# Kernel optimization log

Hardware: AMD Instinct MI355X
Metric: run time of the kernel (lower is better)

The kernel has to match this reference:

```python
import jax, jax.numpy as jnp
import numpy as np

DIN = 256
N_RATIOS = 3          # cfg.ANCHOR_RATIOS = [0.5, 1, 2]
NC_SCORE = N_RATIOS * 2   # 6
NC_BBOX = N_RATIOS * 4    # 12
LEVEL_SHAPES = [(150, 250), (75, 125), (38, 63), (19, 32), (10, 16)]


def setup_inputs() -> dict:
    key = jax.random.key(0)
    ks = jax.random.split(key, 12)
    inp = {}
    for i, (h, w) in enumerate(LEVEL_SHAPES):
        inp[f"rpn_feat_p{i+2}"] = jax.random.normal(ks[i], (4, DIN, h, w), dtype=jnp.float32)
    inp["im_info"] = jnp.ones((4, 3), dtype=jnp.float32)
    s = 0.01
    inp["W_conv"] = jax.random.normal(ks[5], (512, DIN, 3, 3), dtype=jnp.float32) * s
    inp["b_conv"] = jnp.zeros((512,), dtype=jnp.float32)
    inp["W_cls"] = jax.random.normal(ks[6], (NC_SCORE, 512), dtype=jnp.float32) * s
    inp["b_cls"] = jnp.zeros((NC_SCORE,), dtype=jnp.float32)
    inp["W_box"] = jax.random.normal(ks[7], (NC_BBOX, 512), dtype=jnp.float32) * s
    inp["b_box"] = jnp.zeros((NC_BBOX,), dtype=jnp.float32)
    return inp


def _conv3x3(x, W, b):
    y = jax.lax.conv_general_dilated(
        x, W, window_strides=(1, 1), padding="SAME",
        dimension_numbers=("NCHW", "OIHW", "NCHW"))
    return y + b[None, :, None, None]


def _level_head(feat, W_conv, b_conv, W_cls, b_cls, W_box, b_box):
    B = feat.shape[0]
    conv1 = jax.nn.relu(_conv3x3(feat, W_conv, b_conv))            # [B,512,H,W]
    score = jnp.einsum("bchw,oc->bohw", conv1, W_cls) + b_cls[None, :, None, None]  # [B,6,H,W]
    bbox = jnp.einsum("bchw,oc->bohw", conv1, W_box) + b_box[None, :, None, None]   # [B,12,H,W]
    _, C, H, W = score.shape
    # reshape(x, 2): view(B, 2, C*H/2, W), softmax over dim 1, reshape back
    prob = jax.nn.softmax(score.reshape(B, 2, (C * H) // 2, W), axis=1).reshape(B, C, H, W)
    score_f = score.transpose(0, 2, 3, 1).reshape(B, -1, 2)
    prob_f = prob.transpose(0, 2, 3, 1).reshape(B, -1, 2)
    bbox_f = bbox.transpose(0, 2, 3, 1).reshape(B, -1, 4)
    return score_f, prob_f, bbox_f


def reference(rpn_feat_p2, rpn_feat_p3, rpn_feat_p4, rpn_feat_p5, rpn_feat_p6,
              im_info, W_conv, b_conv, W_cls, b_cls, W_box, b_box):
    feats = [rpn_feat_p2, rpn_feat_p3, rpn_feat_p4, rpn_feat_p5, rpn_feat_p6]
    scores, probs, boxes = [], [], []
    for f in feats:  # fixed 5 FPN levels
        s, p, b = _level_head(f, W_conv, b_conv, W_cls, b_cls, W_box, b_box)
        scores.append(s); probs.append(p); boxes.append(b)
    rpn_cls_score_alls = jnp.concatenate(scores, axis=1)            # [B, N, 2]
    rpn_cls_prob_alls = jnp.concatenate(probs, axis=1)              # [B, N, 2]
    rpn_bbox_pred_alls = jnp.concatenate(boxes, axis=1)             # [B, N, 4]
    return rpn_cls_score_alls, rpn_cls_prob_alls, rpn_bbox_pred_alls
```

## Files before the change

kernel.cpp:

```cpp
#include <hip/hip_runtime.h>
#include <stdint.h>


typedef __bf16 bf16x8 __attribute__((ext_vector_type(8)));
typedef float  f32x4  __attribute__((ext_vector_type(4)));

#define WS_WR2_OFF   0
#define WS_WH2_OFF   2359296
#define WS_SB_OFF    2392064
#define WS_FP_OFF    17100800
#define WS_TOTAL     123197440

__device__ __forceinline__ unsigned short f2bf(float f) {
    unsigned u = __builtin_bit_cast(unsigned, f);
    unsigned r = (u + 0x7FFF + ((u >> 16) & 1)) >> 16;
    return (unsigned short)r;
}

__device__ __forceinline__ void gl_lds16(const void* g, void* l) {
    __builtin_amdgcn_global_load_lds(
        (const __attribute__((address_space(1))) unsigned int*)g,
        (__attribute__((address_space(3))) unsigned int*)l, 16, 0, 0);
}

__global__ __launch_bounds__(256) void prep_weights(
    const float* __restrict__ Wc, const float* __restrict__ Wcls,
    const float* __restrict__ Wbox,
    unsigned short* __restrict__ wr2, unsigned short* __restrict__ wh2)
{
    int idx = blockIdx.x * 256 + threadIdx.x;
    if (idx < 1179648) {
        int o = idx / 2304;
        int k = idx - o * 2304;
        int r = k >> 8, c = k & 255;
        wr2[idx] = f2bf(Wc[o * 2304 + c * 9 + r]);
    } else {
        int i2 = idx - 1179648;
        if (i2 < 16384) {
            int j = i2 >> 9, o = i2 & 511;
            float v = (j < 6) ? Wcls[j * 512 + o]
                    : (j < 18) ? Wbox[(j - 6) * 512 + o] : 0.0f;
            wh2[j * 512 + o] = f2bf(v);
        }
    }
}

__global__ __launch_bounds__(256) void zero_rings(unsigned short* __restrict__ fpad)
{
    int idx = blockIdx.x * 256 + threadIdx.x;
    int b = idx / 50432;
    int rem = idx - b * 50432;
    int Wp, H, W; long lb;
    if (rem < 25728)      {               Wp=252; H=150; W=250; lb=32768    + (long)b*9805824; }
    else if (rem < 38656) { rem -= 25728; Wp=127; H=75;  W=125; lb=39288832 + (long)b*2503424; }
    else if (rem < 45248) { rem -= 38656; Wp=65;  H=38;  W=63;  lb=49335296 + (long)b*665600;  }
    else if (rem < 48640) { rem -= 45248; Wp=34;  H=19;  W=32;  lb=52030464 + (long)b*182784;  }
    else                  { rem -= 48640; Wp=18;  H=10;  W=16;  lb=52794368 + (long)b*55296;   }
    int c = rem >> 5, slot = rem & 31;
    int h, w;
    if (c < Wp)          { h = 0;     w = c; }
    else if (c < 2 * Wp) { h = H + 1; w = c - Wp; }
    else {
        int c2 = c - 2 * Wp;
        h = 1 + (c2 >> 1);
        w = (c2 & 1) ? (W + 1) : 0;
    }
    uint4 z = {0u, 0u, 0u, 0u};
    *(uint4*)(fpad + lb + (long)(h * Wp + w) * 256 + slot * 8) = z;
}

__global__ __launch_bounds__(256) void prep_feats(
    const float* __restrict__ f0, const float* __restrict__ f1,
    const float* __restrict__ f2, const float* __restrict__ f3,
    const float* __restrict__ f4, unsigned short* __restrict__ fpad)
{
    __shared__ unsigned short lds[64 * 258];
    int bi = blockIdx.x;
    int b = bi / 817;
    int r = bi - b * 817;
    const float* fsrc; int H, W, Wp, h, wb; long lb;
    if (r < 600)      { fsrc=f0; H=150; W=250; Wp=252; h=r>>2; wb=r&3; lb=32768    + (long)b*9805824; }
    else if (r < 750) { int rr=r-600; fsrc=f1; H=75; W=125; Wp=127; h=rr>>1; wb=rr&1; lb=39288832 + (long)b*2503424; }
    else if (r < 788) { fsrc=f2; H=38; W=63; Wp=65; h=r-750; wb=0; lb=49335296 + (long)b*665600; }
    else if (r < 807) { fsrc=f3; H=19; W=32; Wp=34; h=r-788; wb=0; lb=52030464 + (long)b*182784; }
    else              { fsrc=f4; H=10; W=16; Wp=18; h=r-807; wb=0; lb=52794368 + (long)b*55296; }
    const int t = threadIdx.x;
    const long cstr = (long)H * W;
    const int w = t & 63;
    const int wg = wb * 64 + w;
    const bool wv = (wg < W);
    const float* src = fsrc + (((long)b * 256) * H + h) * W + wg;
    unsigned* ldsw = (unsigned*)lds;
    #pragma unroll 4
    for (int it = 0; it < 32; ++it) {
        int c0 = (t >> 6) * 2 + it * 8;
        float v0 = wv ? src[(long)c0 * cstr] : 0.0f;
        float v1 = wv ? src[(long)(c0 + 1) * cstr] : 0.0f;
        unsigned pk = (unsigned)f2bf(v0) | ((unsigned)f2bf(v1) << 16);
        ldsw[w * 129 + (c0 >> 1)] = pk;
    }
    __syncthreads();
    #pragma unroll
    for (int k = 0; k < 8; ++k) {
        int g  = k * 256 + t;
        int px = g >> 5;
        int pg = wb * 64 + px;
        if (pg >= W) continue;
        int d0 = px * 129 + (g & 31) * 4;
        uint4 v;
        v.x = ldsw[d0]; v.y = ldsw[d0 + 1]; v.z = ldsw[d0 + 2]; v.w = ldsw[d0 + 3];
        unsigned short* dst = fpad + lb + (long)((h + 1) * Wp + (pg + 1)) * 256 + (g & 31) * 8;
        *(uint4*)dst = v;
    }
}

__global__ __launch_bounds__(256) void conv_main(
    const unsigned short* __restrict__ fpad,
    const unsigned short* __restrict__ wr2,
    const unsigned short* __restrict__ wh2,
    const float* __restrict__ b_conv,
    float* __restrict__ sbuf)
{
    __shared__ unsigned short smem[16384];
    const int tid = threadIdx.x;
    const int bid = blockIdx.x;
    const int tile = ((bid >> 5) << 3) + (bid & 7);
    const int chunk = (bid >> 3) & 3;
    if (tile >= 1596) return;
    int b = tile / 399;
    int tr = tile - b * 399;
    int Wp, lt; long lb;
    if (tr < 296)      { lt = tr;       Wp = 252; lb = 32768    + (long)b * 9805824; }
    else if (tr < 371) { lt = tr - 296; Wp = 127; lb = 39288832 + (long)b * 2503424; }
    else if (tr < 391) { lt = tr - 371; Wp = 65;  lb = 49335296 + (long)b * 665600;  }
    else if (tr < 397) { lt = tr - 391; Wp = 34;  lb = 52030464 + (long)b * 182784;  }
    else               { lt = tr - 397; Wp = 18;  lb = 52794368 + (long)b * 55296;   }

    const int arow  = tid >> 3;
    const int aslot = (tid & 7) ^ (arow & 7);
    const long apix = lb + (long)(Wp + lt * 128 + arow) * 256 + aslot * 8;
    const long bofs = (long)(chunk * 128 + arow) * 2304 + aslot * 8;

    const int wv = tid >> 6, lane = tid & 63;
    char* lA = (char*)smem + wv * 1024;
    char* lB = (char*)smem + 16384 + wv * 1024;
    const int mrow = (wv & 1) * 64, ncol = (wv >> 1) * 64;
    const int mr = lane & 15;
    const int kq = (lane >> 4) * 8;
    const int m7 = mr & 7;

    f32x4 acc[4][4];
    #pragma unroll
    for (int mt = 0; mt < 4; ++mt)
        #pragma unroll
        for (int nt = 0; nt < 4; ++nt) acc[mt][nt] = (f32x4){0.f, 0.f, 0.f, 0.f};

    for (int r = 0; r < 9; ++r) {
        const int doff = (r / 3 - 1) * Wp + (r % 3 - 1);
        const unsigned short* ga = fpad + apix + (long)doff * 256;
        const unsigned short* gb = wr2 + bofs + r * 256;
        for (int cb = 0; cb < 4; ++cb) {
            const unsigned short* ga2 = ga + cb * 64;
            const unsigned short* gb2 = gb + cb * 64;
            #pragma unroll
            for (int i = 0; i < 4; ++i) {
                gl_lds16(ga2 + i * 8192,  lA + i * 4096);
                gl_lds16(gb2 + i * 73728, lB + i * 4096);
            }
            __syncthreads();
            #pragma unroll
            for (int kk = 0; kk < 64; kk += 32) {
                const int sx = ((((kk >> 3) + (lane >> 4)) ^ m7) << 3);
                bf16x8 af[4], bfr[4];
                #pragma unroll
                for (int mt = 0; mt < 4; ++mt)
                    af[mt] = *(const bf16x8*)&smem[(mrow + mt * 16 + mr) * 64 + sx];
                #pragma unroll
                for (int nt = 0; nt < 4; ++nt)
                    bfr[nt] = *(const bf16x8*)&smem[8192 + (ncol + nt * 16 + mr) * 64 + sx];
                #pragma unroll
                for (int mt = 0; mt < 4; ++mt)
                    #pragma unroll
                    for (int nt = 0; nt < 4; ++nt)
                        acc[mt][nt] = __builtin_amdgcn_mfma_f32_16x16x32_bf16(
                            af[mt], bfr[nt], acc[mt][nt], 0, 0, 0);
            }
            __syncthreads();
        }
    }

    float bias[4];
    #pragma unroll
    for (int nt = 0; nt < 4; ++nt) bias[nt] = b_conv[chunk * 128 + ncol + nt * 16 + mr];
    #pragma unroll
    for (int mt = 0; mt < 4; ++mt)
        #pragma unroll
        for (int nt = 0; nt < 4; ++nt)
            #pragma unroll
            for (int q = 0; q < 4; ++q) {
                int row = mrow + mt * 16 + (lane >> 4) * 4 + q;
                int col = ncol + nt * 16 + mr;
                int sl  = (col >> 3) ^ (row & 7);
                smem[row * 128 + (sl << 3) + (col & 7)] =
                    f2bf(fmaxf(acc[mt][nt][q] + bias[nt], 0.0f));
            }
    __syncthreads();

    f32x4 acc2[2][2];
    #pragma unroll
    for (int mi = 0; mi < 2; ++mi)
        #pragma unroll
        for (int ni = 0; ni < 2; ++ni) acc2[mi][ni] = (f32x4){0.f, 0.f, 0.f, 0.f};
    #pragma unroll
    for (int ks = 0; ks < 4; ++ks) {
        const int sg = ks * 4 + (lane >> 4);
        bf16x8 ha[2], hb[2];
        #pragma unroll
        for (int mi = 0; mi < 2; ++mi) {
            int rowH = (wv * 2 + mi) * 16 + mr;
            ha[mi] = *(const bf16x8*)&smem[rowH * 128 + ((sg ^ m7) << 3)];
        }
        #pragma unroll
        for (int ni = 0; ni < 2; ++ni)
            hb[ni] = *(const bf16x8*)&wh2[(ni * 16 + mr) * 512 + chunk * 128 + ks * 32 + kq];
        #pragma unroll
        for (int mi = 0; mi < 2; ++mi)
            #pragma unroll
            for (int ni = 0; ni < 2; ++ni)
                acc2[mi][ni] = __builtin_amdgcn_mfma_f32_16x16x32_bf16(
                    ha[mi], hb[ni], acc2[mi][ni], 0, 0, 0);
    }
    const long slotbase = (long)tile * 128;
    #pragma unroll
    for (int ni = 0; ni < 2; ++ni) {
        int j = ni * 16 + mr;
        if (j < 18) {
            #pragma unroll
            for (int mi = 0; mi < 2; ++mi)
                #pragma unroll
                for (int q = 0; q < 4; ++q) {
                    int row = (wv * 2 + mi) * 16 + (lane >> 4) * 4 + q;
                    atomicAdd(&sbuf[(slotbase + row) * 18 + j], acc2[mi][ni][q]);
                }
        }
    }
}

__global__ __launch_bounds__(256) void finalize(
    const float* __restrict__ sbuf, const float* __restrict__ b_cls,
    const float* __restrict__ b_box, float* __restrict__ out)
{
    int idx = blockIdx.x * 256 + threadIdx.x;
    int tile = idx >> 7, m = idx & 127;
    int b = tile / 399;
    int tr = tile - b * 399;
    int hp, wp, H, W, noff;
    if (tr < 296)      { int f = 252 + (tr)       * 128 + m; hp = f / 252; wp = f - hp * 252; H = 150; W = 250; noff = 0; }
    else if (tr < 371) { int f = 127 + (tr - 296) * 128 + m; hp = f / 127; wp = f - hp * 127; H = 75;  W = 125; noff = 112500; }
    else if (tr < 391) { int f = 65  + (tr - 371) * 128 + m; hp = f / 65;  wp = f - hp * 65;  H = 38;  W = 63;  noff = 140625; }
    else if (tr < 397) { int f = 34  + (tr - 391) * 128 + m; hp = f / 34;  wp = f - hp * 34;  H = 19;  W = 32;  noff = 147807; }
    else               { int f = 18  + (tr - 397) * 128 + m; hp = f / 18;  wp = f - hp * 18;  H = 10;  W = 16;  noff = 149631; }
    if (hp < 1 || hp > H || wp < 1 || wp > W) return;

    const float* s = sbuf + (long)idx * 18;
    float sc[6], bb[12], pr[6];
    #pragma unroll
    for (int c = 0; c < 6; ++c) sc[c] = s[c] + b_cls[c];
    #pragma unroll
    for (int k = 0; k < 12; ++k) bb[k] = s[6 + k] + b_box[k];
    #pragma unroll
    for (int c = 0; c < 6; ++c) {
        int p = (c < 3) ? c + 3 : c - 3;
        pr[c] = 1.0f / (1.0f + expf(sc[p] - sc[c]));
    }
    int n = noff + ((hp - 1) * W + (wp - 1)) * 3;
    long o0 = ((long)b * 150111 + n) * 2;
    float* O0 = out + o0;
    float* O1 = out + 1200888 + o0;
    float* O2 = out + 2401776 + ((long)b * 150111 + n) * 4;
    #pragma unroll
    for (int c = 0; c < 6; ++c) { O0[c] = sc[c]; O1[c] = pr[c]; }
    #pragma unroll
    for (int k = 0; k < 12; ++k) O2[k] = bb[k];
}

extern "C" void kernel_launch(void* const* d_in, const int* in_sizes, int n_in,
                              void* d_out, int out_size, void* d_ws, size_t ws_size,
                              hipStream_t stream)
{
    const float* f0   = (const float*)d_in[0];
    const float* f1   = (const float*)d_in[1];
    const float* f2   = (const float*)d_in[2];
    const float* f3   = (const float*)d_in[3];
    const float* f4   = (const float*)d_in[4];
    const float* Wc   = (const float*)d_in[6];
    const float* bC   = (const float*)d_in[7];
    const float* Wcls = (const float*)d_in[8];
    const float* bcls = (const float*)d_in[9];
    const float* Wbox = (const float*)d_in[10];
    const float* bbox = (const float*)d_in[11];

    unsigned short* wr2  = (unsigned short*)((char*)d_ws + WS_WR2_OFF);
    unsigned short* wh2  = (unsigned short*)((char*)d_ws + WS_WH2_OFF);
    float*          sbuf = (float*)((char*)d_ws + WS_SB_OFF);
    unsigned short* fpad = (unsigned short*)((char*)d_ws + WS_FP_OFF);

    hipMemsetAsync((char*)d_ws + WS_SB_OFF, 0, (size_t)(WS_FP_OFF - WS_SB_OFF), stream);
    hipLaunchKernelGGL(prep_weights, dim3(4672), dim3(256), 0, stream, Wc, Wcls, Wbox, wr2, wh2);
    hipLaunchKernelGGL(zero_rings,   dim3(788),  dim3(256), 0, stream, fpad);
    hipLaunchKernelGGL(prep_feats,   dim3(3268), dim3(256), 0, stream, f0, f1, f2, f3, f4, fpad);
    hipLaunchKernelGGL(conv_main,    dim3(6400), dim3(256), 0, stream, fpad, wr2, wh2, bC, sbuf);
    hipLaunchKernelGGL(finalize,     dim3(798),  dim3(256), 0, stream, sbuf, bcls, bbox, (float*)d_out);
}
```

Measured before the change: 886.1 us.

## Fuse head epilogue into conv kernel and merge prep kernels into one

Each conv block now loops over all four output-channel chunks itself, instead of splitting them across blocks. It accumulates the 1x1 head results in registers, stages them in shared memory and applies bias, softmax and the output scatter in-kernel. This removes the float atomics, the scratch-buffer memset and the separate finalize launch. The weight prep, ring zeroing and feature packing kernels are merged into a single launch. The trade-off is four times fewer, longer conv blocks, which can worsen tail balance and lose the previous L2 sharing of input tiles across chunk blocks.

```diff
diff --git a/kernel.cpp b/kernel.cpp
--- a/kernel.cpp
+++ b/kernel.cpp
@@ -7,9 +7,7 @@
 
 #define WS_WR2_OFF   0
 #define WS_WH2_OFF   2359296
-#define WS_SB_OFF    2392064
 #define WS_FP_OFF    17100800
-#define WS_TOTAL     123197440
 
 __device__ __forceinline__ unsigned short f2bf(float f) {
     unsigned u = __builtin_bit_cast(unsigned, f);
@@ -23,20 +21,86 @@
         (__attribute__((address_space(3))) unsigned int*)l, 16, 0, 0);
 }
 
-__global__ __launch_bounds__(256) void prep_weights(
+__global__ __launch_bounds__(256) void prep_all(
+    const float* __restrict__ f0, const float* __restrict__ f1,
+    const float* __restrict__ f2, const float* __restrict__ f3,
+    const float* __restrict__ f4,
     const float* __restrict__ Wc, const float* __restrict__ Wcls,
     const float* __restrict__ Wbox,
+    unsigned short* __restrict__ fpad,
     unsigned short* __restrict__ wr2, unsigned short* __restrict__ wh2)
 {
-    int idx = blockIdx.x * 256 + threadIdx.x;
-    if (idx < 1179648) {
-        int o = idx / 2304;
-        int k = idx - o * 2304;
-        int r = k >> 8, c = k & 255;
-        wr2[idx] = f2bf(Wc[o * 2304 + c * 9 + r]);
+    __shared__ unsigned short lds[64 * 258];
+    const int blk = blockIdx.x;
+    const int t = threadIdx.x;
+
+    if (blk < 3268) {
+        int bi = blk;
+        int b = bi / 817;
+        int r = bi - b * 817;
+        const float* fsrc; int H, W, Wp, h, wb; long lb;
+        if (r < 600)      { fsrc=f0; H=150; W=250; Wp=252; h=r>>2; wb=r&3; lb=32768    + (long)b*9805824; }
+        else if (r < 750) { int rr=r-600; fsrc=f1; H=75; W=125; Wp=127; h=rr>>1; wb=rr&1; lb=39288832 + (long)b*2503424; }
+        else if (r < 788) { fsrc=f2; H=38; W=63; Wp=65; h=r-750; wb=0; lb=49335296 + (long)b*665600; }
+        else if (r < 807) { fsrc=f3; H=19; W=32; Wp=34; h=r-788; wb=0; lb=52030464 + (long)b*182784; }
+        else              { fsrc=f4; H=10; W=16; Wp=18; h=r-807; wb=0; lb=52794368 + (long)b*55296; }
+        const long cstr = (long)H * W;
+        const int w = t & 63;
+        const int wg = wb * 64 + w;
+        const bool wok = (wg < W);
+        const float* src = fsrc + (((long)b * 256) * H + h) * W + wg;
+        unsigned* ldsw = (unsigned*)lds;
+        #pragma unroll 4
+        for (int it = 0; it < 32; ++it) {
+            int c0 = (t >> 6) * 2 + it * 8;
+            float v0 = wok ? src[(long)c0 * cstr] : 0.0f;
+            float v1 = wok ? src[(long)(c0 + 1) * cstr] : 0.0f;
+            unsigned pk = (unsigned)f2bf(v0) | ((unsigned)f2bf(v1) << 16);
+            ldsw[w * 129 + (c0 >> 1)] = pk;
+        }
+        __syncthreads();
+        #pragma unroll
+        for (int k = 0; k < 8; ++k) {
+            int g  = k * 256 + t;
+            int px = g >> 5;
+            int pg = wb * 64 + px;
+            if (pg >= W) continue;
+            int d0 = px * 129 + (g & 31) * 4;
+            uint4 v;
+            v.x = ldsw[d0]; v.y = ldsw[d0 + 1]; v.z = ldsw[d0 + 2]; v.w = ldsw[d0 + 3];
+            unsigned short* dst = fpad + lb + (long)((h + 1) * Wp + (pg + 1)) * 256 + (g & 31) * 8;
+            *(uint4*)dst = v;
+        }
+    } else if (blk < 4056) {
+        int idx = (blk - 3268) * 256 + t;
+        int b = idx / 50432;
+        int rem = idx - b * 50432;
+        int Wp, H, W; long lb;
+        if (rem < 25728)      {               Wp=252; H=150; W=250; lb=32768    + (long)b*9805824; }
+        else if (rem < 38656) { rem -= 25728; Wp=127; H=75;  W=125; lb=39288832 + (long)b*2503424; }
+        else if (rem < 45248) { rem -= 38656; Wp=65;  H=38;  W=63;  lb=49335296 + (long)b*665600;  }
+        else if (rem < 48640) { rem -= 45248; Wp=34;  H=19;  W=32;  lb=52030464 + (long)b*182784;  }
+        else                  { rem -= 48640; Wp=18;  H=10;  W=16;  lb=52794368 + (long)b*55296;   }
+        int c = rem >> 5, slot = rem & 31;
+        int h, w;
+        if (c < Wp)          { h = 0;     w = c; }
+        else if (c < 2 * Wp) { h = H + 1; w = c - Wp; }
+        else {
+            int c2 = c - 2 * Wp;
+            h = 1 + (c2 >> 1);
+            w = (c2 & 1) ? (W + 1) : 0;
+        }
+        uint4 z = {0u, 0u, 0u, 0u};
+        *(uint4*)(fpad + lb + (long)(h * Wp + w) * 256 + slot * 8) = z;
     } else {
-        int i2 = idx - 1179648;
-        if (i2 < 16384) {
+        int idx = (blk - 4056) * 256 + t;
+        if (idx < 1179648) {
+            int o = idx / 2304;
+            int k = idx - o * 2304;
+            int r = k >> 8, c = k & 255;
+            wr2[idx] = f2bf(Wc[o * 2304 + c * 9 + r]);
+        } else {
+            int i2 = idx - 1179648;
             int j = i2 >> 9, o = i2 & 511;
             float v = (j < 6) ? Wcls[j * 512 + o]
                     : (j < 18) ? Wbox[(j - 6) * 512 + o] : 0.0f;
@@ -45,101 +109,31 @@
     }
 }
 
-__global__ __launch_bounds__(256) void zero_rings(unsigned short* __restrict__ fpad)
-{
-    int idx = blockIdx.x * 256 + threadIdx.x;
-    int b = idx / 50432;
-    int rem = idx - b * 50432;
-    int Wp, H, W; long lb;
-    if (rem < 25728)      {               Wp=252; H=150; W=250; lb=32768    + (long)b*9805824; }
-    else if (rem < 38656) { rem -= 25728; Wp=127; H=75;  W=125; lb=39288832 + (long)b*2503424; }
-    else if (rem < 45248) { rem -= 38656; Wp=65;  H=38;  W=63;  lb=49335296 + (long)b*665600;  }
-    else if (rem < 48640) { rem -= 45248; Wp=34;  H=19;  W=32;  lb=52030464 + (long)b*182784;  }
-    else                  { rem -= 48640; Wp=18;  H=10;  W=16;  lb=52794368 + (long)b*55296;   }
-    int c = rem >> 5, slot = rem & 31;
-    int h, w;
-    if (c < Wp)          { h = 0;     w = c; }
-    else if (c < 2 * Wp) { h = H + 1; w = c - Wp; }
-    else {
-        int c2 = c - 2 * Wp;
-        h = 1 + (c2 >> 1);
-        w = (c2 & 1) ? (W + 1) : 0;
-    }
-    uint4 z = {0u, 0u, 0u, 0u};
-    *(uint4*)(fpad + lb + (long)(h * Wp + w) * 256 + slot * 8) = z;
-}
-
-__global__ __launch_bounds__(256) void prep_feats(
-    const float* __restrict__ f0, const float* __restrict__ f1,
-    const float* __restrict__ f2, const float* __restrict__ f3,
-    const float* __restrict__ f4, unsigned short* __restrict__ fpad)
-{
-    __shared__ unsigned short lds[64 * 258];
-    int bi = blockIdx.x;
-    int b = bi / 817;
-    int r = bi - b * 817;
-    const float* fsrc; int H, W, Wp, h, wb; long lb;
-    if (r < 600)      { fsrc=f0; H=150; W=250; Wp=252; h=r>>2; wb=r&3; lb=32768    + (long)b*9805824; }
-    else if (r < 750) { int rr=r-600; fsrc=f1; H=75; W=125; Wp=127; h=rr>>1; wb=rr&1; lb=39288832 + (long)b*2503424; }
-    else if (r < 788) { fsrc=f2; H=38; W=63; Wp=65; h=r-750; wb=0; lb=49335296 + (long)b*665600; }
-    else if (r < 807) { fsrc=f3; H=19; W=32; Wp=34; h=r-788; wb=0; lb=52030464 + (long)b*182784; }
-    else              { fsrc=f4; H=10; W=16; Wp=18; h=r-807; wb=0; lb=52794368 + (long)b*55296; }
-    const int t = threadIdx.x;
-    const long cstr = (long)H * W;
-    const int w = t & 63;
-    const int wg = wb * 64 + w;
-    const bool wv = (wg < W);
-    const float* src = fsrc + (((long)b * 256) * H + h) * W + wg;
-    unsigned* ldsw = (unsigned*)lds;
-    #pragma unroll 4
-    for (int it = 0; it < 32; ++it) {
-        int c0 = (t >> 6) * 2 + it * 8;
-        float v0 = wv ? src[(long)c0 * cstr] : 0.0f;
-        float v1 = wv ? src[(long)(c0 + 1) * cstr] : 0.0f;
-        unsigned pk = (unsigned)f2bf(v0) | ((unsigned)f2bf(v1) << 16);
-        ldsw[w * 129 + (c0 >> 1)] = pk;
-    }
-    __syncthreads();
-    #pragma unroll
-    for (int k = 0; k < 8; ++k) {
-        int g  = k * 256 + t;
-        int px = g >> 5;
-        int pg = wb * 64 + px;
-        if (pg >= W) continue;
-        int d0 = px * 129 + (g & 31) * 4;
-        uint4 v;
-        v.x = ldsw[d0]; v.y = ldsw[d0 + 1]; v.z = ldsw[d0 + 2]; v.w = ldsw[d0 + 3];
-        unsigned short* dst = fpad + lb + (long)((h + 1) * Wp + (pg + 1)) * 256 + (g & 31) * 8;
-        *(uint4*)dst = v;
-    }
-}
-
-__global__ __launch_bounds__(256) void conv_main(
+__global__ __launch_bounds__(256) void conv_fused(
     const unsigned short* __restrict__ fpad,
     const unsigned short* __restrict__ wr2,
     const unsigned short* __restrict__ wh2,
     const float* __restrict__ b_conv,
-    float* __restrict__ sbuf)
+    const float* __restrict__ b_cls,
+    const float* __restrict__ b_box,
+    float* __restrict__ out)
 {
     __shared__ unsigned short smem[16384];
     const int tid = threadIdx.x;
-    const int bid = blockIdx.x;
-    const int tile = ((bid >> 5) << 3) + (bid & 7);
-    const int chunk = (bid >> 3) & 3;
-    if (tile >= 1596) return;
+    const int tile = blockIdx.x;
     int b = tile / 399;
     int tr = tile - b * 399;
-    int Wp, lt; long lb;
-    if (tr < 296)      { lt = tr;       Wp = 252; lb = 32768    + (long)b * 9805824; }
-    else if (tr < 371) { lt = tr - 296; Wp = 127; lb = 39288832 + (long)b * 2503424; }
-    else if (tr < 391) { lt = tr - 371; Wp = 65;  lb = 49335296 + (long)b * 665600;  }
-    else if (tr < 397) { lt = tr - 391; Wp = 34;  lb = 52030464 + (long)b * 182784;  }
-    else               { lt = tr - 397; Wp = 18;  lb = 52794368 + (long)b * 55296;   }
+    int Wp, lt, H, W, noff; long lb;
+    if (tr < 296)      { lt = tr;       Wp=252; H=150; W=250; noff=0;      lb = 32768    + (long)b*9805824; }
+    else if (tr < 371) { lt = tr - 296; Wp=127; H=75;  W=125; noff=112500; lb = 39288832 + (long)b*2503424; }
+    else if (tr < 391) { lt = tr - 371; Wp=65;  H=38;  W=63;  noff=140625; lb = 49335296 + (long)b*665600;  }
+    else if (tr < 397) { lt = tr - 391; Wp=34;  H=19;  W=32;  noff=147807; lb = 52030464 + (long)b*182784;  }
+    else               { lt = tr - 397; Wp=18;  H=10;  W=16;  noff=149631; lb = 52794368 + (long)b*55296;   }
 
     const int arow  = tid >> 3;
     const int aslot = (tid & 7) ^ (arow & 7);
-    const long apix = lb + (long)(Wp + lt * 128 + arow) * 256 + aslot * 8;
-    const long bofs = (long)(chunk * 128 + arow) * 2304 + aslot * 8;
+    const long apix  = lb + (long)(Wp + lt * 128 + arow) * 256 + aslot * 8;
+    const long bofs0 = (long)arow * 2304 + aslot * 8;
 
     const int wv = tid >> 6, lane = tid & 63;
     char* lA = (char*)smem + wv * 1024;
@@ -149,88 +143,94 @@
     const int kq = (lane >> 4) * 8;
     const int m7 = mr & 7;
 
-    f32x4 acc[4][4];
-    #pragma unroll
-    for (int mt = 0; mt < 4; ++mt)
-        #pragma unroll
-        for (int nt = 0; nt < 4; ++nt) acc[mt][nt] = (f32x4){0.f, 0.f, 0.f, 0.f};
-
-    for (int r = 0; r < 9; ++r) {
-        const int doff = (r / 3 - 1) * Wp + (r % 3 - 1);
-        const unsigned short* ga = fpad + apix + (long)doff * 256;
-        const unsigned short* gb = wr2 + bofs + r * 256;
-        for (int cb = 0; cb < 4; ++cb) {
-            const unsigned short* ga2 = ga + cb * 64;
-            const unsigned short* gb2 = gb + cb * 64;
-            #pragma unroll
-            for (int i = 0; i < 4; ++i) {
-                gl_lds16(ga2 + i * 8192,  lA + i * 4096);
-                gl_lds16(gb2 + i * 73728, lB + i * 4096);
-            }
-            __syncthreads();
-            #pragma unroll
-            for (int kk = 0; kk < 64; kk += 32) {
-                const int sx = ((((kk >> 3) + (lane >> 4)) ^ m7) << 3);
-                bf16x8 af[4], bfr[4];
-                #pragma unroll
-                for (int mt = 0; mt < 4; ++mt)
-                    af[mt] = *(const bf16x8*)&smem[(mrow + mt * 16 + mr) * 64 + sx];
-                #pragma unroll
-                for (int nt = 0; nt < 4; ++nt)
-                    bfr[nt] = *(const bf16x8*)&smem[8192 + (ncol + nt * 16 + mr) * 64 + sx];
-                #pragma unroll
-                for (int mt = 0; mt < 4; ++mt)
-                    #pragma unroll
-                    for (int nt = 0; nt < 4; ++nt)
-                        acc[mt][nt] = __builtin_amdgcn_mfma_f32_16x16x32_bf16(
-                            af[mt], bfr[nt], acc[mt][nt], 0, 0, 0);
-            }
-            __syncthreads();
-        }
-    }
-
-    float bias[4];
-    #pragma unroll
-    for (int nt = 0; nt < 4; ++nt) bias[nt] = b_conv[chunk * 128 + ncol + nt * 16 + mr];
-    #pragma unroll
-    for (int mt = 0; mt < 4; ++mt)
-        #pragma unroll
-        for (int nt = 0; nt < 4; ++nt)
-            #pragma unroll
-            for (int q = 0; q < 4; ++q) {
-                int row = mrow + mt * 16 + (lane >> 4) * 4 + q;
-                int col = ncol + nt * 16 + mr;
-                int sl  = (col >> 3) ^ (row & 7);
-                smem[row * 128 + (sl << 3) + (col & 7)] =
-                    f2bf(fmaxf(acc[mt][nt][q] + bias[nt], 0.0f));
-            }
-    __syncthreads();
-
     f32x4 acc2[2][2];
     #pragma unroll
     for (int mi = 0; mi < 2; ++mi)
         #pragma unroll
         for (int ni = 0; ni < 2; ++ni) acc2[mi][ni] = (f32x4){0.f, 0.f, 0.f, 0.f};
-    #pragma unroll
-    for (int ks = 0; ks < 4; ++ks) {
-        const int sg = ks * 4 + (lane >> 4);
-        bf16x8 ha[2], hb[2];
-        #pragma unroll
-        for (int mi = 0; mi < 2; ++mi) {
-            int rowH = (wv * 2 + mi) * 16 + mr;
-            ha[mi] = *(const bf16x8*)&smem[rowH * 128 + ((sg ^ m7) << 3)];
-        }
-        #pragma unroll
-        for (int ni = 0; ni < 2; ++ni)
-            hb[ni] = *(const bf16x8*)&wh2[(ni * 16 + mr) * 512 + chunk * 128 + ks * 32 + kq];
-        #pragma unroll
-        for (int mi = 0; mi < 2; ++mi)
+
+    for (int chunk = 0; chunk < 4; ++chunk) {
+        const unsigned short* wrc = wr2 + (long)chunk * 294912;
+        f32x4 acc[4][4];
+        #pragma unroll
+        for (int mt = 0; mt < 4; ++mt)
+            #pragma unroll
+            for (int nt = 0; nt < 4; ++nt) acc[mt][nt] = (f32x4){0.f, 0.f, 0.f, 0.f};
+
+        for (int r = 0; r < 9; ++r) {
+            const int doff = (r / 3 - 1) * Wp + (r % 3 - 1);
+            const unsigned short* ga = fpad + apix + (long)doff * 256;
+            const unsigned short* gb = wrc + bofs0 + r * 256;
+            for (int cb = 0; cb < 4; ++cb) {
+                const unsigned short* ga2 = ga + cb * 64;
+                const unsigned short* gb2 = gb + cb * 64;
+                #pragma unroll
+                for (int i = 0; i < 4; ++i) {
+                    gl_lds16(ga2 + i * 8192,  lA + i * 4096);
+                    gl_lds16(gb2 + i * 73728, lB + i * 4096);
+                }
+                __syncthreads();
+                #pragma unroll
+                for (int kk = 0; kk < 64; kk += 32) {
+                    const int sx = ((((kk >> 3) + (lane >> 4)) ^ m7) << 3);
+                    bf16x8 af[4], bfr[4];
+                    #pragma unroll
+                    for (int mt = 0; mt < 4; ++mt)
+                        af[mt] = *(const bf16x8*)&smem[(mrow + mt * 16 + mr) * 64 + sx];
+                    #pragma unroll
+                    for (int nt = 0; nt < 4; ++nt)
+                        bfr[nt] = *(const bf16x8*)&smem[8192 + (ncol + nt * 16 + mr) * 64 + sx];
+                    #pragma unroll
+                    for (int mt = 0; mt < 4; ++mt)
+                        #pragma unroll
+                        for (int nt = 0; nt < 4; ++nt)
+                            acc[mt][nt] = __builtin_amdgcn_mfma_f32_16x16x32_bf16(
+                                af[mt], bfr[nt], acc[mt][nt], 0, 0, 0);
+                }
+                __syncthreads();
+            }
+        }
+
+        float bias[4];
+        #pragma unroll
+        for (int nt = 0; nt < 4; ++nt) bias[nt] = b_conv[chunk * 128 + ncol + nt * 16 + mr];
+        #pragma unroll
+        for (int mt = 0; mt < 4; ++mt)
+            #pragma unroll
+            for (int nt = 0; nt < 4; ++nt)
+                #pragma unroll
+                for (int q = 0; q < 4; ++q) {
+                    int row = mrow + mt * 16 + (lane >> 4) * 4 + q;
+                    int col = ncol + nt * 16 + mr;
+                    int sl  = (col >> 3) ^ (row & 7);
+                    smem[row * 128 + (sl << 3) + (col & 7)] =
+                        f2bf(fmaxf(acc[mt][nt][q] + bias[nt], 0.0f));
+                }
+        __syncthreads();
+
+        #pragma unroll
+        for (int ks = 0; ks < 4; ++ks) {
+            const int sg = ks * 4 + (lane >> 4);
+            bf16x8 ha[2], hb[2];
+            #pragma unroll
+            for (int mi = 0; mi < 2; ++mi) {
+                int rowH = (wv * 2 + mi) * 16 + mr;
+                ha[mi] = *(const bf16x8*)&smem[rowH * 128 + ((sg ^ m7) << 3)];
+            }
             #pragma unroll
             for (int ni = 0; ni < 2; ++ni)
-                acc2[mi][ni] = __builtin_amdgcn_mfma_f32_16x16x32_bf16(
-                    ha[mi], hb[ni], acc2[mi][ni], 0, 0, 0);
+                hb[ni] = *(const bf16x8*)&wh2[(ni * 16 + mr) * 512 + chunk * 128 + ks * 32 + kq];
+            #pragma unroll
+            for (int mi = 0; mi < 2; ++mi)
+                #pragma unroll
+                for (int ni = 0; ni < 2; ++ni)
+                    acc2[mi][ni] = __builtin_amdgcn_mfma_f32_16x16x32_bf16(
+                        ha[mi], hb[ni], acc2[mi][ni], 0, 0, 0);
+        }
+        __syncthreads();
     }
-    const long slotbase = (long)tile * 128;
+
+    float* sf = (float*)smem;
     #pragma unroll
     for (int ni = 0; ni < 2; ++ni) {
         int j = ni * 16 + mr;
@@ -239,49 +239,40 @@
             for (int mi = 0; mi < 2; ++mi)
                 #pragma unroll
                 for (int q = 0; q < 4; ++q) {
-                    int row = (wv * 2 + mi) * 16 + (lane >> 4) * 4 + q;
-                    atomicAdd(&sbuf[(slotbase + row) * 18 + j], acc2[mi][ni][q]);
+                    int px = (wv * 2 + mi) * 16 + (lane >> 4) * 4 + q;
+                    sf[px * 19 + j] = acc2[mi][ni][q];
                 }
         }
     }
-}
-
-__global__ __launch_bounds__(256) void finalize(
-    const float* __restrict__ sbuf, const float* __restrict__ b_cls,
-    const float* __restrict__ b_box, float* __restrict__ out)
-{
-    int idx = blockIdx.x * 256 + threadIdx.x;
-    int tile = idx >> 7, m = idx & 127;
-    int b = tile / 399;
-    int tr = tile - b * 399;
-    int hp, wp, H, W, noff;
-    if (tr < 296)      { int f = 252 + (tr)       * 128 + m; hp = f / 252; wp = f - hp * 252; H = 150; W = 250; noff = 0; }
-    else if (tr < 371) { int f = 127 + (tr - 296) * 128 + m; hp = f / 127; wp = f - hp * 127; H = 75;  W = 125; noff = 112500; }
-    else if (tr < 391) { int f = 65  + (tr - 371) * 128 + m; hp = f / 65;  wp = f - hp * 65;  H = 38;  W = 63;  noff = 140625; }
-    else if (tr < 397) { int f = 34  + (tr - 391) * 128 + m; hp = f / 34;  wp = f - hp * 34;  H = 19;  W = 32;  noff = 147807; }
-    else               { int f = 18  + (tr - 397) * 128 + m; hp = f / 18;  wp = f - hp * 18;  H = 10;  W = 16;  noff = 149631; }
-    if (hp < 1 || hp > H || wp < 1 || wp > W) return;
-
-    const float* s = sbuf + (long)idx * 18;
-    float sc[6], bb[12], pr[6];
-    #pragma unroll
-    for (int c = 0; c < 6; ++c) sc[c] = s[c] + b_cls[c];
-    #pragma unroll
-    for (int k = 0; k < 12; ++k) bb[k] = s[6 + k] + b_box[k];
-    #pragma unroll
-    for (int c = 0; c < 6; ++c) {
-        int p = (c < 3) ? c + 3 : c - 3;
-        pr[c] = 1.0f / (1.0f + expf(sc[p] - sc[c]));
+    __syncthreads();
+
+    if (tid < 128) {
+        const int m = tid;
+        const int f = Wp + lt * 128 + m;
+        const int hp = f / Wp, wp = f - hp * Wp;
+        if (hp >= 1 && hp <= H && wp >= 1 && wp <= W) {
+            const float* s = sf + m * 19;
+            float sc[6], bb[12], pr[6];
+            #pragma unroll
+            for (int c = 0; c < 6; ++c) sc[c] = s[c] + b_cls[c];
+            #pragma unroll
+            for (int k = 0; k < 12; ++k) bb[k] = s[6 + k] + b_box[k];
+            #pragma unroll
+            for (int c = 0; c < 6; ++c) {
+                int p = (c < 3) ? c + 3 : c - 3;
+                pr[c] = 1.0f / (1.0f + expf(sc[p] - sc[c]));
+            }
+            int n = noff + ((hp - 1) * W + (wp - 1)) * 3;
+            long o0 = ((long)b * 150111 + n) * 2;
+            float* O0 = out + o0;
+            float* O1 = out + 1200888 + o0;
+            float* O2 = out + 2401776 + ((long)b * 150111 + n) * 4;
+            #pragma unroll
+            for (int c = 0; c < 6; ++c) { O0[c] = sc[c]; O1[c] = pr[c]; }
+            #pragma unroll
+            for (int k = 0; k < 12; ++k) O2[k] = bb[k];
+        }
     }
-    int n = noff + ((hp - 1) * W + (wp - 1)) * 3;
-    long o0 = ((long)b * 150111 + n) * 2;
-    float* O0 = out + o0;
-    float* O1 = out + 1200888 + o0;
-    float* O2 = out + 2401776 + ((long)b * 150111 + n) * 4;
-    #pragma unroll
-    for (int c = 0; c < 6; ++c) { O0[c] = sc[c]; O1[c] = pr[c]; }
-    #pragma unroll
-    for (int k = 0; k < 12; ++k) O2[k] = bb[k];
 }
 
 extern "C" void kernel_launch(void* const* d_in, const int* in_sizes, int n_in,
@@ -302,13 +293,10 @@
 
     unsigned short* wr2  = (unsigned short*)((char*)d_ws + WS_WR2_OFF);
     unsigned short* wh2  = (unsigned short*)((char*)d_ws + WS_WH2_OFF);
-    float*          sbuf = (float*)((char*)d_ws + WS_SB_OFF);
     unsigned short* fpad = (unsigned short*)((char*)d_ws + WS_FP_OFF);
 
-    hipMemsetAsync((char*)d_ws + WS_SB_OFF, 0, (size_t)(WS_FP_OFF - WS_SB_OFF), stream);
-    hipLaunchKernelGGL(prep_weights, dim3(4672), dim3(256), 0, stream, Wc, Wcls, Wbox, wr2, wh2);
-    hipLaunchKernelGGL(zero_rings,   dim3(788),  dim3(256), 0, stream, fpad);
-    hipLaunchKernelGGL(prep_feats,   dim3(3268), dim3(256), 0, stream, f0, f1, f2, f3, f4, fpad);
-    hipLaunchKernelGGL(conv_main,    dim3(6400), dim3(256), 0, stream, fpad, wr2, wh2, bC, sbuf);
-    hipLaunchKernelGGL(finalize,     dim3(798),  dim3(256), 0, stream, sbuf, bcls, bbox, (float*)d_out);
-}
+    hipLaunchKernelGGL(prep_all, dim3(8728), dim3(256), 0, stream,
+                       f0, f1, f2, f3, f4, Wc, Wcls, Wbox, fpad, wr2, wh2);
+    hipLaunchKernelGGL(conv_fused, dim3(1596), dim3(256), 0, stream,
+                       fpad, wr2, wh2, bC, bcls, bbox, (float*)d_out);
+}
```

Result: slower. 1.342 ms (+51.5%).
